# Kernel tuning notes

Hardware: AMD Instinct MI355X
Metric: run time of the kernel (lower is better)

The kernel has to match this reference:

```python
import jax, jax.numpy as jnp
import numpy as np

E, H, I, K, T = 32, 2048, 768, 4, 2048


def setup_inputs() -> dict:
    key = jax.random.key(0)
    k1, k2, k3, k4, k5 = jax.random.split(key, 5)
    hidden_states = jax.random.normal(k1, (T, H), dtype=jnp.float32)
    top_k_index = jax.random.randint(k2, (T, K), 0, E, dtype=jnp.int64)
    top_k_weights = jax.random.uniform(k3, (T, K), dtype=jnp.float32)
    gate_up_proj = jax.random.normal(k4, (E, H, 2 * I), dtype=jnp.float32) * 0.02
    down_proj = jax.random.normal(k5, (E, I, H), dtype=jnp.float32) * 0.02
    return {
        "hidden_states": hidden_states,
        "top_k_index": top_k_index,
        "top_k_weights": top_k_weights,
        "gate_up_proj": gate_up_proj,
        "down_proj": down_proj,
    }


def reference(hidden_states, top_k_index, top_k_weights, gate_up_proj, down_proj):
    # Dense routing-weight matrix [T, E]: zeros scattered with top-k weights
    num_tokens = hidden_states.shape[0]
    routing = jnp.zeros((num_tokens, E), dtype=hidden_states.dtype)
    routing = routing.at[jnp.arange(num_tokens)[:, None], top_k_index].set(top_k_weights)

    # Batched (grouped) GEMM over all experts; weights are stored transposed
    # gate_up_proj: [E, H, 2I] -> gu: [E, T, 2I]
    gu = jnp.einsum('th,ehi->eti', hidden_states, gate_up_proj)
    gate, up = jnp.split(gu, 2, axis=-1)           # each [E, T, I]
    inter = jax.nn.silu(gate) * up                 # [E, T, I]
    # down_proj: [E, I, H] -> per-expert output [E, T, H]
    expert_out = jnp.einsum('eti,eih->eth', inter, down_proj)
    # Weighted combine over experts
    out = jnp.einsum('te,eth->th', routing, expert_out)
    return out
```

## Files before the change

kernel.cpp:

```cpp
#include <hip/hip_runtime.h>
#include <hip/hip_bf16.h>

#define E_ 32
#define H_ 2048
#define I_ 768
#define T_ 2048
#define TWO_I 1536
#define MAX_TILES 96

typedef __attribute__((ext_vector_type(8))) short short8;
typedef __attribute__((ext_vector_type(4))) float floatx4;

#define WS_OFFSETS 0
#define WS_IDS     1024
#define WS_WTS     (1024 + 32768)
#define WS_TILES   (1024 + 65536)
#define WS_INTER   131072
#define WS_HID16   (131072 + 8192*768*2)

__device__ __forceinline__ unsigned short f2bf(float f) {
  union { float f; unsigned u; } v; v.f = f;
  unsigned r = v.u + 0x7FFFu + ((v.u >> 16) & 1u);
  return (unsigned short)(r >> 16);
}

__device__ __forceinline__ unsigned pkbf(float a, float b) {
  __hip_bfloat162 h = __float22bfloat162_rn(float2{a, b});
  union { __hip_bfloat162 h; unsigned u; } v; v.h = h; return v.u;
}

__global__ void build_routing(const int* __restrict__ idx, const float* __restrict__ w,
                              char* __restrict__ ws) {
  int* offs = (int*)(ws + WS_OFFSETS);
  int* ids  = (int*)(ws + WS_IDS);
  float* wt = (float*)(ws + WS_WTS);
  int* tiles = (int*)(ws + WS_TILES);
  __shared__ int s_cnt[E_];
  __shared__ int s_pos[E_];
  int tid = threadIdx.x;
  if (tid < E_) s_cnt[tid] = 0;
  __syncthreads();
  for (int i = tid; i < T_ * 4; i += 256) {
    int t = i >> 2, j = i & 3;
    int e = idx[i];
    bool keep = true;
    for (int j2 = j + 1; j2 < 4; ++j2) if (idx[t * 4 + j2] == e) keep = false;
    if (keep) atomicAdd(&s_cnt[e], 1);
  }
  __syncthreads();
  if (tid == 0) {
    int run = 0;
    for (int e = 0; e < E_; ++e) { offs[e] = run; s_pos[e] = run; run += s_cnt[e]; }
    offs[E_] = run;
    int nt = 0;
    for (int e = 0; e < E_; ++e)
      for (int m0 = 0; m0 < s_cnt[e]; m0 += 128) tiles[nt++] = (e << 16) | (m0 >> 7);
    for (; nt < MAX_TILES; ++nt) tiles[nt] = -1;
  }
  __syncthreads();
  for (int i = tid; i < T_ * 4; i += 256) {
    int t = i >> 2, j = i & 3;
    int e = idx[i];
    bool keep = true;
    for (int j2 = j + 1; j2 < 4; ++j2) if (idx[t * 4 + j2] == e) keep = false;
    if (keep) {
      int p = atomicAdd(&s_pos[e], 1);
      ids[p] = t;
      wt[p] = w[i];
    }
  }
}

__global__ void cvt_hidden(const float* __restrict__ hs, char* __restrict__ ws) {
  int g = blockIdx.x * 256 + threadIdx.x;
  const float4 f0 = ((const float4*)hs)[g * 2];
  const float4 f1 = ((const float4*)hs)[g * 2 + 1];
  uint4 o;
  o.x = pkbf(f0.x, f0.y); o.y = pkbf(f0.z, f0.w);
  o.z = pkbf(f1.x, f1.y); o.w = pkbf(f1.z, f1.w);
  ((uint4*)(ws + WS_HID16))[g] = o;
}

__global__ __launch_bounds__(256, 2) void gemm1(
    const float* __restrict__ gup, char* __restrict__ ws) {
  const int* offs = (const int*)(ws + WS_OFFSETS);
  const int* ids  = (const int*)(ws + WS_IDS);
  const int* tiles = (const int*)(ws + WS_TILES);
  const unsigned short* h16 = (const unsigned short*)(ws + WS_HID16);
  unsigned short* inter = (unsigned short*)(ws + WS_INTER);

  int tl = tiles[blockIdx.y];
  if (tl < 0) return;
  int e = tl >> 16, m0 = (tl & 0xffff) << 7;
  int start = offs[e];
  int mrem = offs[e + 1] - start - m0;
  int n0 = blockIdx.x * 64;

  __shared__ __align__(16) unsigned short Al[128][72];
  __shared__ __align__(16) unsigned short Bl[128][72];

  int tid = threadIdx.x, lane = tid & 63, wid = tid >> 6;
  int wy = wid >> 1, wx = wid & 1, quad = lane >> 4, l15 = lane & 15;

  floatx4 acc[4][4] = {};

  int arow[4], ako[4];
  const unsigned short* asrc[4];
#pragma unroll
  for (int u = 0; u < 4; ++u) {
    int lin = tid + u * 256;
    arow[u] = lin >> 3; ako[u] = (lin & 7) * 8;
    int tok = (arow[u] < mrem) ? ids[start + m0 + arow[u]] : -1;
    asrc[u] = (tok >= 0) ? h16 + (size_t)tok * H_ + ako[u] : nullptr;
  }
  int bj = tid & 127;
  int kr0 = (tid >> 7) * 32;
  int gc = (bj < 64) ? (n0 + bj) : (I_ + n0 + (bj - 64));
  const float* gbase = gup + (size_t)e * H_ * TWO_I + gc;

  uint4 pf_a[4];
  float pf_b[32];

  auto loadA = [&](int kb) {
#pragma unroll
    for (int u = 0; u < 4; ++u)
      pf_a[u] = asrc[u] ? *(const uint4*)(asrc[u] + (size_t)kb * 64) : uint4{0u, 0u, 0u, 0u};
  };
  auto loadB = [&](int kb) {
    const float* p = gbase + (size_t)(kb * 64 + kr0) * TWO_I;
#pragma unroll
    for (int r = 0; r < 32; ++r) pf_b[r] = p[(size_t)r * TWO_I];
  };

  loadA(0); loadB(0);
  for (int kb = 0; kb < H_ / 64; ++kb) {
#pragma unroll
    for (int u = 0; u < 4; ++u) *(uint4*)&Al[arow[u]][ako[u]] = pf_a[u];
#pragma unroll
    for (int q = 0; q < 4; ++q) {
      uint4 wv;
      wv.x = pkbf(pf_b[q * 8 + 0], pf_b[q * 8 + 1]);
      wv.y = pkbf(pf_b[q * 8 + 2], pf_b[q * 8 + 3]);
      wv.z = pkbf(pf_b[q * 8 + 4], pf_b[q * 8 + 5]);
      wv.w = pkbf(pf_b[q * 8 + 6], pf_b[q * 8 + 7]);
      *(uint4*)&Bl[bj][kr0 + q * 8] = wv;
    }
    __syncthreads();
    if (kb + 1 < H_ / 64) { loadA(kb + 1); loadB(kb + 1); }
#pragma unroll
    for (int ks = 0; ks < 2; ++ks) {
      short8 af[4], bfr[4];
#pragma unroll
      for (int mi = 0; mi < 4; ++mi)
        af[mi] = *(const short8*)&Al[wy * 64 + mi * 16 + l15][ks * 32 + quad * 8];
#pragma unroll
      for (int ni = 0; ni < 4; ++ni) {
        int j = (ni < 2) ? (wx * 32 + ni * 16 + l15) : (64 + wx * 32 + (ni - 2) * 16 + l15);
        bfr[ni] = *(const short8*)&Bl[j][ks * 32 + quad * 8];
      }
#pragma unroll
      for (int mi = 0; mi < 4; ++mi)
#pragma unroll
        for (int ni = 0; ni < 4; ++ni)
          acc[mi][ni] = __builtin_amdgcn_mfma_f32_16x16x32_bf16(af[mi], bfr[ni], acc[mi][ni], 0, 0, 0);
    }
    __syncthreads();
  }

#pragma unroll
  for (int mi = 0; mi < 4; ++mi) {
#pragma unroll
    for (int r = 0; r < 4; ++r) {
      int row = wy * 64 + mi * 16 + quad * 4 + r;
      if (row < mrem) {
        int slot = start + m0 + row;
#pragma unroll
        for (int ni = 0; ni < 2; ++ni) {
          float g = acc[mi][ni][r];
          float u = acc[mi][ni + 2][r];
          float s = g / (1.f + __expf(-g));
          int col = n0 + wx * 32 + ni * 16 + l15;
          inter[(size_t)slot * I_ + col] = f2bf(s * u);
        }
      }
    }
  }
}

__global__ __launch_bounds__(256, 2) void gemm2(
    const float* __restrict__ down, float* __restrict__ out, char* __restrict__ ws) {
  const int* offs = (const int*)(ws + WS_OFFSETS);
  const int* ids  = (const int*)(ws + WS_IDS);
  const float* wt = (const float*)(ws + WS_WTS);
  const int* tiles = (const int*)(ws + WS_TILES);
  const unsigned short* inter = (const unsigned short*)(ws + WS_INTER);

  int tl = tiles[blockIdx.y];
  if (tl < 0) return;
  int e = tl >> 16, m0 = (tl & 0xffff) << 7;
  int start = offs[e];
  int mrem = offs[e + 1] - start - m0;
  int n0 = blockIdx.x * 128;

  __shared__ __align__(16) unsigned short Al[128][72];
  __shared__ __align__(16) unsigned short Bl[128][72];

  int tid = threadIdx.x, lane = tid & 63, wid = tid >> 6;
  int wy = wid >> 1, wx = wid & 1, quad = lane >> 4, l15 = lane & 15;

  floatx4 acc[4][4] = {};

  int arow[4], ako[4];
  const unsigned short* asrc[4];
#pragma unroll
  for (int u = 0; u < 4; ++u) {
    int lin = tid + u * 256;
    arow[u] = lin >> 3; ako[u] = (lin & 7) * 8;
    asrc[u] = (arow[u] < mrem) ? inter + (size_t)(start + m0 + arow[u]) * I_ + ako[u] : nullptr;
  }
  int bj = tid & 127;
  int kr0 = (tid >> 7) * 32;
  const float* dbase = down + (size_t)e * I_ * H_ + (n0 + bj);

  uint4 pf_a[4];
  float pf_b[32];

  auto loadA = [&](int kb) {
#pragma unroll
    for (int u = 0; u < 4; ++u)
      pf_a[u] = asrc[u] ? *(const uint4*)(asrc[u] + (size_t)kb * 64) : uint4{0u, 0u, 0u, 0u};
  };
  auto loadB = [&](int kb) {
    const float* p = dbase + (size_t)(kb * 64 + kr0) * H_;
#pragma unroll
    for (int r = 0; r < 32; ++r) pf_b[r] = p[(size_t)r * H_];
  };

  loadA(0); loadB(0);
  for (int kb = 0; kb < I_ / 64; ++kb) {
#pragma unroll
    for (int u = 0; u < 4; ++u) *(uint4*)&Al[arow[u]][ako[u]] = pf_a[u];
#pragma unroll
    for (int q = 0; q < 4; ++q) {
      uint4 wv;
      wv.x = pkbf(pf_b[q * 8 + 0], pf_b[q * 8 + 1]);
      wv.y = pkbf(pf_b[q * 8 + 2], pf_b[q * 8 + 3]);
      wv.z = pkbf(pf_b[q * 8 + 4], pf_b[q * 8 + 5]);
      wv.w = pkbf(pf_b[q * 8 + 6], pf_b[q * 8 + 7]);
      *(uint4*)&Bl[bj][kr0 + q * 8] = wv;
    }
    __syncthreads();
    if (kb + 1 < I_ / 64) { loadA(kb + 1); loadB(kb + 1); }
#pragma unroll
    for (int ks = 0; ks < 2; ++ks) {
      short8 af[4], bfr[4];
#pragma unroll
      for (int mi = 0; mi < 4; ++mi)
        af[mi] = *(const short8*)&Al[wy * 64 + mi * 16 + l15][ks * 32 + quad * 8];
#pragma unroll
      for (int ni = 0; ni < 4; ++ni)
        bfr[ni] = *(const short8*)&Bl[wx * 64 + ni * 16 + l15][ks * 32 + quad * 8];
#pragma unroll
      for (int mi = 0; mi < 4; ++mi)
#pragma unroll
        for (int ni = 0; ni < 4; ++ni)
          acc[mi][ni] = __builtin_amdgcn_mfma_f32_16x16x32_bf16(af[mi], bfr[ni], acc[mi][ni], 0, 0, 0);
    }
    __syncthreads();
  }

#pragma unroll
  for (int mi = 0; mi < 4; ++mi) {
#pragma unroll
    for (int r = 0; r < 4; ++r) {
      int row = wy * 64 + mi * 16 + quad * 4 + r;
      if (row < mrem) {
        int slot = start + m0 + row;
        int t = ids[slot];
        float w = wt[slot];
#pragma unroll
        for (int ni = 0; ni < 4; ++ni) {
          int col = n0 + wx * 64 + ni * 16 + l15;
          atomicAdd(out + (size_t)t * H_ + col, w * acc[mi][ni][r]);
        }
      }
    }
  }
}

extern "C" void kernel_launch(void* const* d_in, const int* in_sizes, int n_in,
                              void* d_out, int out_size, void* d_ws, size_t ws_size,
                              hipStream_t stream) {
  (void)in_sizes; (void)n_in; (void)out_size; (void)ws_size;
  const float* hidden = (const float*)d_in[0];
  const int* idx      = (const int*)d_in[1];
  const float* w      = (const float*)d_in[2];
  const float* gup    = (const float*)d_in[3];
  const float* down   = (const float*)d_in[4];
  float* out = (float*)d_out;
  char* ws = (char*)d_ws;

  hipMemsetAsync(d_out, 0, (size_t)T_ * H_ * sizeof(float), stream);
  build_routing<<<1, 256, 0, stream>>>(idx, w, ws);
  cvt_hidden<<<T_ * H_ / 8 / 256, 256, 0, stream>>>(hidden, ws);
  gemm1<<<dim3(I_ / 64, MAX_TILES), 256, 0, stream>>>(gup, ws);
  gemm2<<<dim3(H_ / 128, MAX_TILES), 256, 0, stream>>>(down, out, ws);
}
```

Before: 820.3 us.

## Pre-transpose expert weights to bf16 and stream tiles via global_load_lds

Adds a transpose-and-convert pass that writes gate_up and down weights as K-contiguous bf16 into a large workspace region. New GEMM kernels then load A and B tiles directly into swizzled LDS with global_load_lds, instead of converting fp32 weights inside the GEMM. This is meant to cut weight conversion work and register staging in the main loops, at the cost of an extra full read and write of all expert weights on every call. The new path runs only when the workspace is large enough; otherwise the old kernels are used.

```diff
diff --git a/kernel.cpp b/kernel.cpp
--- a/kernel.cpp
+++ b/kernel.cpp
@@ -17,6 +17,9 @@
 #define WS_TILES   (1024 + 65536)
 #define WS_INTER   131072
 #define WS_HID16   (131072 + 8192*768*2)
+#define WS_GUPT    21102592ULL
+#define WS_DOWNT   222429184ULL
+#define WS_BIG_TOTAL 323092480ULL
 
 __device__ __forceinline__ unsigned short f2bf(float f) {
   union { float f; unsigned u; } v; v.f = f;
@@ -27,6 +30,12 @@
 __device__ __forceinline__ unsigned pkbf(float a, float b) {
   __hip_bfloat162 h = __float22bfloat162_rn(float2{a, b});
   union { __hip_bfloat162 h; unsigned u; } v; v.h = h; return v.u;
+}
+
+__device__ __forceinline__ void gload_lds16(const unsigned short* g, unsigned short* l) {
+  __builtin_amdgcn_global_load_lds(
+      (__attribute__((address_space(1))) void*)g,
+      (__attribute__((address_space(3))) void*)l, 16, 0, 0);
 }
 
 __global__ void build_routing(const int* __restrict__ idx, const float* __restrict__ w,
@@ -81,7 +90,212 @@
   ((uint4*)(ws + WS_HID16))[g] = o;
 }
 
-__global__ __launch_bounds__(256, 2) void gemm1(
+template<int R, int C>
+__global__ void tconv(const float* __restrict__ in, unsigned short* __restrict__ outp) {
+  __shared__ float tile[64][65];
+  int e = blockIdx.z;
+  int rb = blockIdx.y * 64, cb = blockIdx.x * 64;
+  const float* src = in + (size_t)e * R * C;
+  unsigned short* dst = outp + (size_t)e * R * C;
+  int t = threadIdx.x;
+  int tr = t >> 4, tc4 = t & 15;
+#pragma unroll
+  for (int p = 0; p < 4; ++p) {
+    int r = p * 16 + tr;
+    const float4 v = *(const float4*)(src + (size_t)(rb + r) * C + cb + tc4 * 4);
+    tile[r][tc4 * 4 + 0] = v.x;
+    tile[r][tc4 * 4 + 1] = v.y;
+    tile[r][tc4 * 4 + 2] = v.z;
+    tile[r][tc4 * 4 + 3] = v.w;
+  }
+  __syncthreads();
+  int c0 = t >> 3, r0 = (t & 7) * 8;
+#pragma unroll
+  for (int q = 0; q < 2; ++q) {
+    int c = q * 32 + c0;
+    uint4 o;
+    o.x = pkbf(tile[r0 + 0][c], tile[r0 + 1][c]);
+    o.y = pkbf(tile[r0 + 2][c], tile[r0 + 3][c]);
+    o.z = pkbf(tile[r0 + 4][c], tile[r0 + 5][c]);
+    o.w = pkbf(tile[r0 + 6][c], tile[r0 + 7][c]);
+    *(uint4*)(dst + (size_t)(cb + c) * R + rb + r0) = o;
+  }
+}
+
+
+__global__ __launch_bounds__(256, 3) void gemm1_bf(char* __restrict__ ws) {
+  const int* offs = (const int*)(ws + WS_OFFSETS);
+  const int* ids  = (const int*)(ws + WS_IDS);
+  const int* tiles = (const int*)(ws + WS_TILES);
+  const unsigned short* h16  = (const unsigned short*)(ws + WS_HID16);
+  const unsigned short* gupT = (const unsigned short*)(ws + WS_GUPT);
+  unsigned short* inter = (unsigned short*)(ws + WS_INTER);
+
+  int tl = tiles[blockIdx.y];
+  if (tl < 0) return;
+  int e = tl >> 16, m0 = (tl & 0xffff) << 7;
+  int start = offs[e];
+  int mrem = offs[e + 1] - start - m0;
+  int n0 = blockIdx.x * 64;
+
+  __shared__ __align__(16) unsigned short Al[128 * 64];
+  __shared__ __align__(16) unsigned short Bl[128 * 64];
+
+  int tid = threadIdx.x, lane = tid & 63, w = tid >> 6;
+  int wy = w >> 1, wx = w & 1, quad = lane >> 4, l15 = lane & 15;
+
+  const unsigned short* aSrc[4];
+  const unsigned short* bSrc[4];
+#pragma unroll
+  for (int u = 0; u < 4; ++u) {
+    int s = (w * 4 + u) * 64 + lane;
+    int r = s >> 3;
+    int c = (s & 7) ^ (r & 7);
+    int tok = ids[start + m0 + ((r < mrem) ? r : 0)];
+    aSrc[u] = h16 + (size_t)tok * H_ + c * 8;
+    int grow = (r < 64) ? (n0 + r) : (I_ + n0 + (r - 64));
+    bSrc[u] = gupT + ((size_t)e * TWO_I + grow) * H_ + c * 8;
+  }
+
+  floatx4 acc[4][4] = {};
+
+  for (int kb = 0; kb < H_ / 64; ++kb) {
+#pragma unroll
+    for (int u = 0; u < 4; ++u) {
+      gload_lds16(aSrc[u] + kb * 64, &Al[(w * 4 + u) * 512]);
+      gload_lds16(bSrc[u] + kb * 64, &Bl[(w * 4 + u) * 512]);
+    }
+    __syncthreads();
+#pragma unroll
+    for (int ks = 0; ks < 2; ++ks) {
+      short8 af[4], bfr[4];
+#pragma unroll
+      for (int mi = 0; mi < 4; ++mi) {
+        int row = wy * 64 + mi * 16 + l15;
+        int c16 = (ks * 4 + quad) ^ (row & 7);
+        af[mi] = *(const short8*)&Al[row * 64 + c16 * 8];
+      }
+#pragma unroll
+      for (int ni = 0; ni < 4; ++ni) {
+        int j = (ni < 2) ? (wx * 32 + ni * 16 + l15) : (64 + wx * 32 + (ni - 2) * 16 + l15);
+        int c16 = (ks * 4 + quad) ^ (j & 7);
+        bfr[ni] = *(const short8*)&Bl[j * 64 + c16 * 8];
+      }
+#pragma unroll
+      for (int mi = 0; mi < 4; ++mi)
+#pragma unroll
+        for (int ni = 0; ni < 4; ++ni)
+          acc[mi][ni] = __builtin_amdgcn_mfma_f32_16x16x32_bf16(af[mi], bfr[ni], acc[mi][ni], 0, 0, 0);
+    }
+    __syncthreads();
+  }
+
+#pragma unroll
+  for (int mi = 0; mi < 4; ++mi) {
+#pragma unroll
+    for (int r = 0; r < 4; ++r) {
+      int row = wy * 64 + mi * 16 + quad * 4 + r;
+      if (row < mrem) {
+        int slot = start + m0 + row;
+#pragma unroll
+        for (int ni = 0; ni < 2; ++ni) {
+          float g = acc[mi][ni][r];
+          float u = acc[mi][ni + 2][r];
+          float s = g / (1.f + __expf(-g));
+          int col = n0 + wx * 32 + ni * 16 + l15;
+          inter[(size_t)slot * I_ + col] = f2bf(s * u);
+        }
+      }
+    }
+  }
+}
+
+__global__ __launch_bounds__(256, 3) void gemm2_bf(float* __restrict__ out, char* __restrict__ ws) {
+  const int* offs = (const int*)(ws + WS_OFFSETS);
+  const int* ids  = (const int*)(ws + WS_IDS);
+  const float* wt = (const float*)(ws + WS_WTS);
+  const int* tiles = (const int*)(ws + WS_TILES);
+  const unsigned short* inter = (const unsigned short*)(ws + WS_INTER);
+  const unsigned short* downT = (const unsigned short*)(ws + WS_DOWNT);
+
+  int tl = tiles[blockIdx.y];
+  if (tl < 0) return;
+  int e = tl >> 16, m0 = (tl & 0xffff) << 7;
+  int start = offs[e];
+  int mrem = offs[e + 1] - start - m0;
+  int n0 = blockIdx.x * 128;
+
+  __shared__ __align__(16) unsigned short Al[128 * 64];
+  __shared__ __align__(16) unsigned short Bl[128 * 64];
+
+  int tid = threadIdx.x, lane = tid & 63, w = tid >> 6;
+  int wy = w >> 1, wx = w & 1, quad = lane >> 4, l15 = lane & 15;
+
+  const unsigned short* aSrc[4];
+  const unsigned short* bSrc[4];
+#pragma unroll
+  for (int u = 0; u < 4; ++u) {
+    int s = (w * 4 + u) * 64 + lane;
+    int r = s >> 3;
+    int c = (s & 7) ^ (r & 7);
+    int arow = (r < mrem) ? r : 0;
+    aSrc[u] = inter + (size_t)(start + m0 + arow) * I_ + c * 8;
+    bSrc[u] = downT + ((size_t)e * H_ + (n0 + r)) * I_ + c * 8;
+  }
+
+  floatx4 acc[4][4] = {};
+
+  for (int kb = 0; kb < I_ / 64; ++kb) {
+#pragma unroll
+    for (int u = 0; u < 4; ++u) {
+      gload_lds16(aSrc[u] + kb * 64, &Al[(w * 4 + u) * 512]);
+      gload_lds16(bSrc[u] + kb * 64, &Bl[(w * 4 + u) * 512]);
+    }
+    __syncthreads();
+#pragma unroll
+    for (int ks = 0; ks < 2; ++ks) {
+      short8 af[4], bfr[4];
+#pragma unroll
+      for (int mi = 0; mi < 4; ++mi) {
+        int row = wy * 64 + mi * 16 + l15;
+        int c16 = (ks * 4 + quad) ^ (row & 7);
+        af[mi] = *(const short8*)&Al[row * 64 + c16 * 8];
+      }
+#pragma unroll
+      for (int ni = 0; ni < 4; ++ni) {
+        int j = wx * 64 + ni * 16 + l15;
+        int c16 = (ks * 4 + quad) ^ (j & 7);
+        bfr[ni] = *(const short8*)&Bl[j * 64 + c16 * 8];
+      }
+#pragma unroll
+      for (int mi = 0; mi < 4; ++mi)
+#pragma unroll
+        for (int ni = 0; ni < 4; ++ni)
+          acc[mi][ni] = __builtin_amdgcn_mfma_f32_16x16x32_bf16(af[mi], bfr[ni], acc[mi][ni], 0, 0, 0);
+    }
+    __syncthreads();
+  }
+
+#pragma unroll
+  for (int mi = 0; mi < 4; ++mi) {
+#pragma unroll
+    for (int r = 0; r < 4; ++r) {
+      int row = wy * 64 + mi * 16 + quad * 4 + r;
+      if (row < mrem) {
+        int slot = start + m0 + row;
+        int t = ids[slot];
+        float wv = wt[slot];
+#pragma unroll
+        for (int ni = 0; ni < 4; ++ni) {
+          int col = n0 + wx * 64 + ni * 16 + l15;
+          atomicAdd(out + (size_t)t * H_ + col, wv * acc[mi][ni][r]);
+        }
+      }
+    }
+  }
+}
+
+__global__ __launch_bounds__(256, 2) void gemm1_fb(
     const float* __restrict__ gup, char* __restrict__ ws) {
   const int* offs = (const int*)(ws + WS_OFFSETS);
   const int* ids  = (const int*)(ws + WS_IDS);
@@ -187,7 +401,7 @@
   }
 }
 
-__global__ __launch_bounds__(256, 2) void gemm2(
+__global__ __launch_bounds__(256, 2) void gemm2_fb(
     const float* __restrict__ down, float* __restrict__ out, char* __restrict__ ws) {
   const int* offs = (const int*)(ws + WS_OFFSETS);
   const int* ids  = (const int*)(ws + WS_IDS);
@@ -291,7 +505,7 @@
 extern "C" void kernel_launch(void* const* d_in, const int* in_sizes, int n_in,
                               void* d_out, int out_size, void* d_ws, size_t ws_size,
                               hipStream_t stream) {
-  (void)in_sizes; (void)n_in; (void)out_size; (void)ws_size;
+  (void)in_sizes; (void)n_in; (void)out_size;
   const float* hidden = (const float*)d_in[0];
   const int* idx      = (const int*)d_in[1];
   const float* w      = (const float*)d_in[2];
@@ -303,6 +517,16 @@
   hipMemsetAsync(d_out, 0, (size_t)T_ * H_ * sizeof(float), stream);
   build_routing<<<1, 256, 0, stream>>>(idx, w, ws);
   cvt_hidden<<<T_ * H_ / 8 / 256, 256, 0, stream>>>(hidden, ws);
-  gemm1<<<dim3(I_ / 64, MAX_TILES), 256, 0, stream>>>(gup, ws);
-  gemm2<<<dim3(H_ / 128, MAX_TILES), 256, 0, stream>>>(down, out, ws);
-}
+
+  if (ws_size >= WS_BIG_TOTAL) {
+    unsigned short* gupT  = (unsigned short*)(ws + WS_GUPT);
+    unsigned short* downT = (unsigned short*)(ws + WS_DOWNT);
+    tconv<2048, 1536><<<dim3(1536 / 64, 2048 / 64, E_), 256, 0, stream>>>(gup, gupT);
+    tconv<768, 2048><<<dim3(2048 / 64, 768 / 64, E_), 256, 0, stream>>>(down, downT);
+    gemm1_bf<<<dim3(I_ / 64, MAX_TILES), 256, 0, stream>>>(ws);
+    gemm2_bf<<<dim3(H_ / 128, MAX_TILES), 256, 0, stream>>>(out, ws);
+  } else {
+    gemm1_fb<<<dim3(I_ / 64, MAX_TILES), 256, 0, stream>>>(gup, ws);
+    gemm2_fb<<<dim3(H_ / 128, MAX_TILES), 256, 0, stream>>>(down, out, ws);
+  }
+}
```

After: 927.4 us. +13.1%, slower.

## Vectorize weight loads with swizzled LDS and replace atomic scatter with combine kernel

Applied to the files above, without the earlier changes.

The B-operand loads in both GEMMs now read float4 rows from two adjacent k-rows instead of 32 scalar strided loads per thread. Each pair is packed into bf16 and written into an XOR-swizzled LDS layout, which is meant to keep the MFMA fragment reads free of bank conflicts. The second GEMM now writes weighted per-slot outputs to a workspace buffer instead of doing float atomicAdd into the output. A new combine kernel sums up to four slots per token, which removes the output memset and the atomics. The cost is an extra intermediate buffer of about 8192x2048 floats that must be written and read back.

```diff
diff --git a/kernel.cpp b/kernel.cpp
--- a/kernel.cpp
+++ b/kernel.cpp
@@ -15,8 +15,10 @@
 #define WS_IDS     1024
 #define WS_WTS     (1024 + 32768)
 #define WS_TILES   (1024 + 65536)
+#define WS_SLOTTJ  69632
 #define WS_INTER   131072
 #define WS_HID16   (131072 + 8192*768*2)
+#define WS_EO      21102592ULL
 
 __device__ __forceinline__ unsigned short f2bf(float f) {
   union { float f; unsigned u; } v; v.f = f;
@@ -35,6 +37,7 @@
   int* ids  = (int*)(ws + WS_IDS);
   float* wt = (float*)(ws + WS_WTS);
   int* tiles = (int*)(ws + WS_TILES);
+  int* slot_tj = (int*)(ws + WS_SLOTTJ);
   __shared__ int s_cnt[E_];
   __shared__ int s_pos[E_];
   int tid = threadIdx.x;
@@ -67,6 +70,9 @@
       int p = atomicAdd(&s_pos[e], 1);
       ids[p] = t;
       wt[p] = w[i];
+      slot_tj[i] = p;
+    } else {
+      slot_tj[i] = -1;
     }
   }
 }
@@ -113,13 +119,21 @@
     int tok = (arow[u] < mrem) ? ids[start + m0 + arow[u]] : -1;
     asrc[u] = (tok >= 0) ? h16 + (size_t)tok * H_ + ako[u] : nullptr;
   }
-  int bj = tid & 127;
-  int kr0 = (tid >> 7) * 32;
-  int gc = (bj < 64) ? (n0 + bj) : (I_ + n0 + (bj - 64));
-  const float* gbase = gup + (size_t)e * H_ * TWO_I + gc;
+  const float* gB[4];
+  int brow0[4], bofs[4];
+#pragma unroll
+  for (int pp = 0; pp < 4; ++pp) {
+    int lin2 = tid + 256 * pp;
+    int k2 = lin2 >> 5, c4 = lin2 & 31;
+    int gcol = (c4 < 16) ? (n0 + c4 * 4) : (I_ + n0 + (c4 - 16) * 4);
+    gB[pp] = gup + (size_t)e * H_ * TWO_I + (size_t)(2 * k2) * TWO_I + gcol;
+    brow0[pp] = c4 * 4;
+    int chunkp = (k2 >> 2) ^ (c4 & 7);
+    bofs[pp] = chunkp * 8 + (k2 & 3) * 2;
+  }
 
   uint4 pf_a[4];
-  float pf_b[32];
+  float4 pf0[4], pf1[4];
 
   auto loadA = [&](int kb) {
 #pragma unroll
@@ -127,9 +141,12 @@
       pf_a[u] = asrc[u] ? *(const uint4*)(asrc[u] + (size_t)kb * 64) : uint4{0u, 0u, 0u, 0u};
   };
   auto loadB = [&](int kb) {
-    const float* p = gbase + (size_t)(kb * 64 + kr0) * TWO_I;
-#pragma unroll
-    for (int r = 0; r < 32; ++r) pf_b[r] = p[(size_t)r * TWO_I];
+#pragma unroll
+    for (int pp = 0; pp < 4; ++pp) {
+      const float* p = gB[pp] + (size_t)kb * 64 * TWO_I;
+      pf0[pp] = *(const float4*)p;
+      pf1[pp] = *(const float4*)(p + TWO_I);
+    }
   };
 
   loadA(0); loadB(0);
@@ -137,13 +154,11 @@
 #pragma unroll
     for (int u = 0; u < 4; ++u) *(uint4*)&Al[arow[u]][ako[u]] = pf_a[u];
 #pragma unroll
-    for (int q = 0; q < 4; ++q) {
-      uint4 wv;
-      wv.x = pkbf(pf_b[q * 8 + 0], pf_b[q * 8 + 1]);
-      wv.y = pkbf(pf_b[q * 8 + 2], pf_b[q * 8 + 3]);
-      wv.z = pkbf(pf_b[q * 8 + 4], pf_b[q * 8 + 5]);
-      wv.w = pkbf(pf_b[q * 8 + 6], pf_b[q * 8 + 7]);
-      *(uint4*)&Bl[bj][kr0 + q * 8] = wv;
+    for (int pp = 0; pp < 4; ++pp) {
+      *(unsigned*)&Bl[brow0[pp] + 0][bofs[pp]] = pkbf(pf0[pp].x, pf1[pp].x);
+      *(unsigned*)&Bl[brow0[pp] + 1][bofs[pp]] = pkbf(pf0[pp].y, pf1[pp].y);
+      *(unsigned*)&Bl[brow0[pp] + 2][bofs[pp]] = pkbf(pf0[pp].z, pf1[pp].z);
+      *(unsigned*)&Bl[brow0[pp] + 3][bofs[pp]] = pkbf(pf0[pp].w, pf1[pp].w);
     }
     __syncthreads();
     if (kb + 1 < H_ / 64) { loadA(kb + 1); loadB(kb + 1); }
@@ -156,7 +171,8 @@
 #pragma unroll
       for (int ni = 0; ni < 4; ++ni) {
         int j = (ni < 2) ? (wx * 32 + ni * 16 + l15) : (64 + wx * 32 + (ni - 2) * 16 + l15);
-        bfr[ni] = *(const short8*)&Bl[j][ks * 32 + quad * 8];
+        int ch = (ks * 4 + quad) ^ ((j >> 2) & 7);
+        bfr[ni] = *(const short8*)&Bl[j][ch * 8];
       }
 #pragma unroll
       for (int mi = 0; mi < 4; ++mi)
@@ -188,12 +204,12 @@
 }
 
 __global__ __launch_bounds__(256, 2) void gemm2(
-    const float* __restrict__ down, float* __restrict__ out, char* __restrict__ ws) {
+    const float* __restrict__ down, char* __restrict__ ws) {
   const int* offs = (const int*)(ws + WS_OFFSETS);
-  const int* ids  = (const int*)(ws + WS_IDS);
   const float* wt = (const float*)(ws + WS_WTS);
   const int* tiles = (const int*)(ws + WS_TILES);
   const unsigned short* inter = (const unsigned short*)(ws + WS_INTER);
+  float* eo = (float*)(ws + WS_EO);
 
   int tl = tiles[blockIdx.y];
   if (tl < 0) return;
@@ -218,12 +234,20 @@
     arow[u] = lin >> 3; ako[u] = (lin & 7) * 8;
     asrc[u] = (arow[u] < mrem) ? inter + (size_t)(start + m0 + arow[u]) * I_ + ako[u] : nullptr;
   }
-  int bj = tid & 127;
-  int kr0 = (tid >> 7) * 32;
-  const float* dbase = down + (size_t)e * I_ * H_ + (n0 + bj);
+  const float* gB[4];
+  int brow0[4], bofs[4];
+#pragma unroll
+  for (int pp = 0; pp < 4; ++pp) {
+    int lin2 = tid + 256 * pp;
+    int k2 = lin2 >> 5, c4 = lin2 & 31;
+    gB[pp] = down + (size_t)e * I_ * H_ + (size_t)(2 * k2) * H_ + (n0 + c4 * 4);
+    brow0[pp] = c4 * 4;
+    int chunkp = (k2 >> 2) ^ (c4 & 7);
+    bofs[pp] = chunkp * 8 + (k2 & 3) * 2;
+  }
 
   uint4 pf_a[4];
-  float pf_b[32];
+  float4 pf0[4], pf1[4];
 
   auto loadA = [&](int kb) {
 #pragma unroll
@@ -231,9 +255,12 @@
       pf_a[u] = asrc[u] ? *(const uint4*)(asrc[u] + (size_t)kb * 64) : uint4{0u, 0u, 0u, 0u};
   };
   auto loadB = [&](int kb) {
-    const float* p = dbase + (size_t)(kb * 64 + kr0) * H_;
-#pragma unroll
-    for (int r = 0; r < 32; ++r) pf_b[r] = p[(size_t)r * H_];
+#pragma unroll
+    for (int pp = 0; pp < 4; ++pp) {
+      const float* p = gB[pp] + (size_t)kb * 64 * H_;
+      pf0[pp] = *(const float4*)p;
+      pf1[pp] = *(const float4*)(p + H_);
+    }
   };
 
   loadA(0); loadB(0);
@@ -241,13 +268,11 @@
 #pragma unroll
     for (int u = 0; u < 4; ++u) *(uint4*)&Al[arow[u]][ako[u]] = pf_a[u];
 #pragma unroll
-    for (int q = 0; q < 4; ++q) {
-      uint4 wv;
-      wv.x = pkbf(pf_b[q * 8 + 0], pf_b[q * 8 + 1]);
-      wv.y = pkbf(pf_b[q * 8 + 2], pf_b[q * 8 + 3]);
-      wv.z = pkbf(pf_b[q * 8 + 4], pf_b[q * 8 + 5]);
-      wv.w = pkbf(pf_b[q * 8 + 6], pf_b[q * 8 + 7]);
-      *(uint4*)&Bl[bj][kr0 + q * 8] = wv;
+    for (int pp = 0; pp < 4; ++pp) {
+      *(unsigned*)&Bl[brow0[pp] + 0][bofs[pp]] = pkbf(pf0[pp].x, pf1[pp].x);
+      *(unsigned*)&Bl[brow0[pp] + 1][bofs[pp]] = pkbf(pf0[pp].y, pf1[pp].y);
+      *(unsigned*)&Bl[brow0[pp] + 2][bofs[pp]] = pkbf(pf0[pp].z, pf1[pp].z);
+      *(unsigned*)&Bl[brow0[pp] + 3][bofs[pp]] = pkbf(pf0[pp].w, pf1[pp].w);
     }
     __syncthreads();
     if (kb + 1 < I_ / 64) { loadA(kb + 1); loadB(kb + 1); }
@@ -258,8 +283,11 @@
       for (int mi = 0; mi < 4; ++mi)
         af[mi] = *(const short8*)&Al[wy * 64 + mi * 16 + l15][ks * 32 + quad * 8];
 #pragma unroll
-      for (int ni = 0; ni < 4; ++ni)
-        bfr[ni] = *(const short8*)&Bl[wx * 64 + ni * 16 + l15][ks * 32 + quad * 8];
+      for (int ni = 0; ni < 4; ++ni) {
+        int j = wx * 64 + ni * 16 + l15;
+        int ch = (ks * 4 + quad) ^ ((j >> 2) & 7);
+        bfr[ni] = *(const short8*)&Bl[j][ch * 8];
+      }
 #pragma unroll
       for (int mi = 0; mi < 4; ++mi)
 #pragma unroll
@@ -276,16 +304,33 @@
       int row = wy * 64 + mi * 16 + quad * 4 + r;
       if (row < mrem) {
         int slot = start + m0 + row;
-        int t = ids[slot];
-        float w = wt[slot];
+        float wv = wt[slot];
 #pragma unroll
         for (int ni = 0; ni < 4; ++ni) {
           int col = n0 + wx * 64 + ni * 16 + l15;
-          atomicAdd(out + (size_t)t * H_ + col, w * acc[mi][ni][r]);
+          eo[(size_t)slot * H_ + col] = wv * acc[mi][ni][r];
         }
       }
     }
   }
+}
+
+__global__ void combine(float* __restrict__ out, const char* __restrict__ ws) {
+  const int* slot_tj = (const int*)(ws + WS_SLOTTJ);
+  const float* eo = (const float*)(ws + WS_EO);
+  int g = blockIdx.x * 256 + threadIdx.x;
+  int token = g >> 9, c4 = g & 511;
+  const int* st = slot_tj + token * 4;
+  float4 s = {0.f, 0.f, 0.f, 0.f};
+#pragma unroll
+  for (int j = 0; j < 4; ++j) {
+    int p = st[j];
+    if (p >= 0) {
+      const float4 v = *(const float4*)(eo + (size_t)p * H_ + c4 * 4);
+      s.x += v.x; s.y += v.y; s.z += v.z; s.w += v.w;
+    }
+  }
+  *(float4*)(out + (size_t)token * H_ + c4 * 4) = s;
 }
 
 extern "C" void kernel_launch(void* const* d_in, const int* in_sizes, int n_in,
@@ -300,9 +345,9 @@
   float* out = (float*)d_out;
   char* ws = (char*)d_ws;
 
-  hipMemsetAsync(d_out, 0, (size_t)T_ * H_ * sizeof(float), stream);
   build_routing<<<1, 256, 0, stream>>>(idx, w, ws);
   cvt_hidden<<<T_ * H_ / 8 / 256, 256, 0, stream>>>(hidden, ws);
   gemm1<<<dim3(I_ / 64, MAX_TILES), 256, 0, stream>>>(gup, ws);
-  gemm2<<<dim3(H_ / 128, MAX_TILES), 256, 0, stream>>>(down, out, ws);
-}
+  gemm2<<<dim3(H_ / 128, MAX_TILES), 256, 0, stream>>>(down, ws);
+  combine<<<T_ * H_ / 4 / 256, 256, 0, stream>>>(out, ws);
+}
```

Result: faster. 799.6 us (-2.5%).
